# Optimization experiments

Measured on AMD Instinct MI355X. Metric: run time of the kernel, lower is better.

Reference implementation:

```python
import jax, jax.numpy as jnp
import numpy as np

NEIGHBOUR = 3  # matches init_kwargs['neighbour']


def _conv2d(x, w, b=None, stride=1, pad=0):
    out = jax.lax.conv_general_dilated(
        x, w, (stride, stride), [(pad, pad), (pad, pad)],
        dimension_numbers=('NCHW', 'OIHW', 'NCHW'))
    if b is not None:
        out = out + b[None, :, None, None]
    return out


def _warp(x, offset, wg_w, wg_b, conv_w):
    """Deformable bilinear warp: offsets -> 4 corner gathers -> modulate -> regroup -> strided conv."""
    k = NEIGHBOUR
    N = k * k
    B, C, H, W = x.shape
    m = jax.nn.sigmoid(_conv2d(x, wg_w, wg_b, 1, 1))          # [B,N,H,W] modulation gate
    xp = jnp.pad(x, ((0, 0), (0, 0), (1, 1), (1, 1)))         # zero pad -> [B,C,H+2,W+2]
    Hp, Wp = H + 2, W + 2
    r = jnp.arange(-(k - 1) // 2, (k - 1) // 2 + 1, dtype=x.dtype)
    pnx, pny = jnp.meshgrid(r, r, indexing='ij')              # kernel-neighbour offsets p_n
    # absolute sampling positions in padded coords (p_0 starts at 1 due to padding)
    p0x = jnp.arange(1, H + 1, dtype=x.dtype)[None, :, None, None]
    p0y = jnp.arange(1, W + 1, dtype=x.dtype)[None, None, :, None]
    off = offset.transpose(0, 2, 3, 1)                        # [B,H,W,2N]; first N = x, last N = y
    px = p0x + pnx.ravel()[None, None, None, :] + off[..., :N]  # [B,H,W,N]
    py = p0y + pny.ravel()[None, None, None, :] + off[..., N:]
    fx = jnp.floor(jax.lax.stop_gradient(px))                 # p.detach().floor()
    fy = jnp.floor(jax.lax.stop_gradient(py))
    qx_lt = jnp.clip(fx, 0, Hp - 1)
    qy_lt = jnp.clip(fy, 0, Wp - 1)
    qx_rb = jnp.clip(fx + 1, 0, Hp - 1)
    qy_rb = jnp.clip(fy + 1, 0, Wp - 1)
    px = jnp.clip(px, 0, Hp - 1)
    py = jnp.clip(py, 0, Wp - 1)
    # bilinear weights (same algebra as the torch code)
    g_lt = (1 + (qx_lt - px)) * (1 + (qy_lt - py))
    g_rb = (1 - (qx_rb - px)) * (1 - (qy_rb - py))
    g_lb = (1 + (qx_lt - px)) * (1 - (qy_rb - py))
    g_rt = (1 - (qx_rb - px)) * (1 + (qy_lt - py))
    ix_lt = qx_lt.astype(jnp.int32); iy_lt = qy_lt.astype(jnp.int32)
    ix_rb = qx_rb.astype(jnp.int32); iy_rb = qy_rb.astype(jnp.int32)
    x_flat = xp.reshape(B, C, Hp * Wp)

    def gather(ix, iy):
        idx = (ix * Wp + iy).reshape(B, 1, H * W * N)
        return jnp.take_along_axis(x_flat, idx, axis=-1).reshape(B, C, H, W, N)

    xw = (g_lt[:, None] * gather(ix_lt, iy_lt)
          + g_rb[:, None] * gather(ix_rb, iy_rb)
          + g_lb[:, None] * gather(ix_lt, iy_rb)
          + g_rt[:, None] * gather(ix_rb, iy_lt))              # [B,C,H,W,N]
    xw = xw * m.transpose(0, 2, 3, 1)[:, None]                 # modulation, broadcast over C
    # regroup [B,C,H,W,k,k] -> [B,C,H*k,W*k] (matches _reshape_x_warped ordering)
    xw = xw.reshape(B, C, H, W, k, k).transpose(0, 1, 2, 4, 3, 5).reshape(B, C, H * k, W * k)
    return _conv2d(xw, conv_w, None, stride=k, pad=0)          # grouped-back strided conv


def setup_inputs() -> dict:
    B, C, MH, H, W = 4, 64, 18, 128, 128  # MH = 2*neighbour^2
    key = jax.random.key(0)
    ks = jax.random.split(key, 12)
    f32 = jnp.float32
    s = 0.05  # weight scale to keep gates unsaturated
    return {
        'x_t': jax.random.normal(ks[0], (B, C, H, W), f32),
        'pre_offset': jax.random.normal(ks[1], (B, MH, H, W), f32),
        'mean': jax.random.normal(ks[2], (B, MH, H, W), f32),
        'upd_w': s * jax.random.normal(ks[3], (MH, C + MH, 3, 3), f32),
        'upd_b': s * jax.random.normal(ks[4], (MH,), f32),
        'rst_w': s * jax.random.normal(ks[5], (MH, C + MH, 3, 3), f32),
        'rst_b': s * jax.random.normal(ks[6], (MH,), f32),
        'out_w': s * jax.random.normal(ks[7], (MH, C + MH, 3, 3), f32),
        'out_b': s * jax.random.normal(ks[8], (MH,), f32),
        'wg_w': s * jax.random.normal(ks[9], (9, C, 3, 3), f32),
        'wg_b': s * jax.random.normal(ks[10], (9,), f32),
        'warp_conv_w': s * jax.random.normal(ks[11], (C, C, 3, 3), f32),
    }


def reference(x_t, pre_offset, mean, upd_w, upd_b, rst_w, rst_b, out_w, out_b,
              wg_w, wg_b, warp_conv_w):
    stacked = jnp.concatenate([x_t, pre_offset], axis=1)
    update_gate = jax.nn.sigmoid(_conv2d(stacked, upd_w, upd_b, 1, 1))
    reset_gate = jax.nn.sigmoid(_conv2d(stacked, rst_w, rst_b, 1, 1))
    cand = jnp.tanh(_conv2d(jnp.concatenate([x_t, pre_offset * reset_gate], axis=1), out_w, out_b, 1, 1))
    offset = pre_offset * (1 - update_gate) + cand * update_gate
    mean_new = mean + 0.5 * (pre_offset - mean)
    offset = offset + mean_new
    x_out = _warp(x_t, offset, wg_w, wg_b, warp_conv_w)
    return (x_out, offset, mean_new)
```

## Files before the change

kernel.cpp:

```cpp
#include <hip/hip_runtime.h>
#include <hip/hip_bf16.h>
#include <math.h>

#define Bn  4
#define Cc  64
#define MHc 18
#define Hh  128
#define Wd  128
#define HW  (Hh*Wd)
#define Np  9
#define HP  130
#define WP  130
#define XPE (HP*WP*Cc)
#define PPE (HP*WP*32)
#define KX  576
#define KP  288
#define KT  (KX+KP)

typedef __attribute__((ext_vector_type(8))) short short8;
typedef __attribute__((ext_vector_type(4))) float float4v;

__device__ __forceinline__ float bf2f(__hip_bfloat16 x) { return __bfloat162float(x); }
__device__ __forceinline__ __hip_bfloat16 f2bf(float x) { return __float2bfloat16(x); }
__device__ __forceinline__ float sigm(float x) { return 1.f / (1.f + expf(-x)); }
__device__ __forceinline__ float s2f(short s) {
  return __uint_as_float(((unsigned)(unsigned short)s) << 16);
}
__device__ __forceinline__ short f2bs(float x) {
  __hip_bfloat16 h = __float2bfloat16(x);
  return *reinterpret_cast<short*>(&h);
}

#define NW1 (64*KT)
#define NW2 (32*KP)
#define NW3 (Cc*Cc*Np)

__global__ __launch_bounds__(256)
void k_prep(const float* __restrict__ x, const float* __restrict__ po,
            const float* __restrict__ upd_w, const float* __restrict__ rst_w,
            const float* __restrict__ out_w, const float* __restrict__ wg_w,
            const float* __restrict__ wcw,
            __hip_bfloat16* __restrict__ xp, __hip_bfloat16* __restrict__ pp,
            __hip_bfloat16* __restrict__ wall, __hip_bfloat16* __restrict__ w2,
            __hip_bfloat16* __restrict__ wt) {
  __shared__ float tile[16][65];
  int blk = blockIdx.x;
  int t = threadIdx.x;
  if (blk < 4096) {
    int wtile = blk & 7;
    int h = (blk >> 3) & 127;
    int b = blk >> 10;
    int w0 = wtile * 16;
    int wa = t & 15, cq = t >> 4;
    #pragma unroll
    for (int j = 0; j < 4; ++j) {
      int c = cq * 4 + j;
      tile[wa][c] = x[(b*Cc + c)*HW + h*Wd + w0 + wa];
    }
    __syncthreads();
    int cb = t & 63, wq = t >> 6;
    #pragma unroll
    for (int j = 0; j < 4; ++j) {
      int w = wq * 4 + j;
      xp[b*XPE + ((h+1)*WP + (w0 + w + 1))*Cc + cb] = f2bf(tile[w][cb]);
    }
  } else if (blk < 4608) {
    int pb = blk - 4096;
    int h = pb & 127;
    int b = pb >> 7;
    int w = t & 127;
    int half = t >> 7;
    for (int j = 0; j < 9; ++j) {
      int ch = half * 9 + j;
      float v = po[(b*MHc + ch)*HW + h*Wd + w];
      pp[b*PPE + ((h+1)*WP + (w+1))*32 + ch] = f2bf(v);
    }
  } else {
    int idx = (blk - 4608) * 256 + t;
    if (idx < NW1) {
      int k  = idx % KT;
      int gr = idx / KT;
      float v = 0.f;
      if (k < KX) {
        int n = k >> 6, ci = k & 63;
        if      (gr < 18) v = upd_w[(gr*(Cc+MHc) + ci)*9 + n];
        else if (gr < 36) v = rst_w[((gr-18)*(Cc+MHc) + ci)*9 + n];
        else if (gr < 54) v = out_w[((gr-36)*(Cc+MHc) + ci)*9 + n];
        else if (gr < 63) v = wg_w[((gr-54)*Cc + ci)*9 + n];
      } else {
        int kk = k - KX;
        int n = kk >> 5, jc = kk & 31;
        if (jc < 18) {
          if      (gr < 18) v = upd_w[(gr*(Cc+MHc) + Cc + jc)*9 + n];
          else if (gr < 36) v = rst_w[((gr-18)*(Cc+MHc) + Cc + jc)*9 + n];
        }
      }
      wall[idx] = f2bf(v);
    } else if (idx < NW1 + NW2) {
      int i2 = idx - NW1;
      int k  = i2 % KP;
      int oc = i2 / KP;
      int n = k >> 5, jc = k & 31;
      float v = (oc < 18 && jc < 18) ? out_w[(oc*(Cc+MHc) + Cc + jc)*9 + n] : 0.f;
      w2[i2] = f2bf(v);
    } else if (idx < NW1 + NW2 + NW3) {
      int i3 = idx - NW1 - NW2;
      int k  = i3 % 576;
      int co = i3 / 576;
      wt[i3] = f2bf(wcw[(co*Cc + (k & 63))*9 + (k >> 6)]);
    }
  }
}

__global__ __launch_bounds__(256)
void k_gates(const __hip_bfloat16* __restrict__ xpad,
             const __hip_bfloat16* __restrict__ popad,
             const __hip_bfloat16* __restrict__ wall,
             const float* __restrict__ po,
             const float* __restrict__ upd_b,
             const float* __restrict__ rst_b,
             const float* __restrict__ out_b,
             const float* __restrict__ wg_b,
             float* __restrict__ u_out,
             float* __restrict__ cx_out,
             __hip_bfloat16* __restrict__ ropad,
             __hip_bfloat16* __restrict__ m_t) {
  __shared__ __align__(16) char winx[6912];
  __shared__ __align__(16) char winp[3456];
  __shared__ __align__(16) __hip_bfloat16 roL[16][32];
  int blk = blockIdx.x;
  int wtile = blk & 7;
  int h = (blk >> 3) & 127;
  int b = blk >> 10;
  int w0 = wtile * 16;
  int lane = threadIdx.x & 63;
  int wave = threadIdx.x >> 6;
  int t = threadIdx.x;

  ((unsigned int*)roL)[t] = 0u;

  const __hip_bfloat16* xpb = xpad + b * XPE;
  const __hip_bfloat16* ppb = popad + b * PPE;

  for (int i = t; i < 432; i += 256) {
    int r = i / 144, cidx = i - r * 144;
    short8 v = *reinterpret_cast<const short8*>(
        xpb + ((h + r) * WP + w0) * Cc + cidx * 8);
    int o = i * 16;
    *reinterpret_cast<short8*>(winx + (o ^ (((o >> 7) & 7) << 4))) = v;
  }
  if (t < 216) {
    int r = t / 72, cidx = t - r * 72;
    short8 v = *reinterpret_cast<const short8*>(
        ppb + ((h + r) * WP + w0) * 32 + cidx * 8);
    int o = t * 16;
    *reinterpret_cast<short8*>(winp + (o ^ (((o >> 6) & 3) << 4))) = v;
  }
  __syncthreads();

  int mrow = lane & 15;
  int quad = lane >> 4;
  int cotile = wave * 16;
  float4v acc = {0.f, 0.f, 0.f, 0.f};
  #pragma unroll
  for (int ks = 0; ks < KT/32; ++ks) {
    short8 a = *reinterpret_cast<const short8*>(
        wall + (cotile + mrow) * KT + ks * 32 + quad * 8);
    short8 bfr;
    if (ks < 18) {
      int n = ks >> 1;
      int rowidx = (n / 3) * 18 + mrow + (n % 3);
      int lin = rowidx * 128 + (ks & 1) * 64 + quad * 16;
      bfr = *reinterpret_cast<const short8*>(winx + (lin ^ ((rowidx & 7) << 4)));
    } else {
      int n = ks - 18;
      int rowidx = (n / 3) * 18 + mrow + (n % 3);
      int lin = rowidx * 64 + quad * 16;
      bfr = *reinterpret_cast<const short8*>(winp + (lin ^ ((rowidx & 3) << 4)));
    }
    acc = __builtin_amdgcn_mfma_f32_16x16x32_bf16(a, bfr, acc, 0, 0, 0);
  }

  int sp = h * Wd + w0 + mrow;
  #pragma unroll
  for (int r = 0; r < 4; ++r) {
    int gr = cotile + quad * 4 + r;
    float v = acc[r];
    if (gr < 18) {
      u_out[(b*MHc + gr)*HW + sp] = sigm(v + upd_b[gr]);
    } else if (gr < 36) {
      int oc = gr - 18;
      float rr = sigm(v + rst_b[oc]);
      roL[mrow][oc] = f2bf(rr * po[(b*MHc + oc)*HW + sp]);
    } else if (gr < 54) {
      int oc = gr - 36;
      cx_out[(b*MHc + oc)*HW + sp] = v + out_b[oc];
    } else if (gr < 63) {
      int nn = gr - 54;
      m_t[(b*HW + sp)*9 + nn] = f2bf(sigm(v + wg_b[nn]));
    }
  }
  __syncthreads();
  unsigned int* dst = (unsigned int*)(ropad + b*PPE + ((h+1)*WP + (w0+1))*32);
  dst[t] = ((unsigned int*)roL)[t];
}

__global__ __launch_bounds__(256)
void k_fuse(const __hip_bfloat16* __restrict__ xpad,
            const __hip_bfloat16* __restrict__ ropad,
            const __hip_bfloat16* __restrict__ w2,
            const __hip_bfloat16* __restrict__ wt,
            const __hip_bfloat16* __restrict__ m_t,
            const float* __restrict__ po,
            const float* __restrict__ mean,
            float* __restrict__ out_off,
            float* __restrict__ out_mn,
            float* __restrict__ out_x) {
  __shared__ __align__(16) char lbuf[16*584*2];
  __shared__ float offL[16][18];
  __shared__ float mL[16][9];
  __shared__ __align__(16) float gw[144][4];
  __shared__ __align__(16) int   gb[144][2];
  auto xw = (__hip_bfloat16(*)[584])lbuf;

  int blk = blockIdx.x;
  int wtile = blk & 7;
  int h = (blk >> 3) & 127;
  int b = blk >> 10;
  int w0 = wtile * 16;
  int lane = threadIdx.x & 63;
  int wave = threadIdx.x >> 6;
  int t = threadIdx.x;

  const __hip_bfloat16* rpb = ropad + b * PPE;
  if (t < 216) {
    int r = t / 72, cidx = t - r * 72;
    short8 v = *reinterpret_cast<const short8*>(
        rpb + ((h + r) * WP + w0) * 32 + cidx * 8);
    int o = t * 16;
    *reinterpret_cast<short8*>(lbuf + (o ^ (((o >> 6) & 3) << 4))) = v;
  }
  __syncthreads();

  int mrow = lane & 15;
  int quad = lane >> 4;

  if (wave < 2) {
    float4v acc = {0.f, 0.f, 0.f, 0.f};
    #pragma unroll
    for (int ks = 0; ks < KP/32; ++ks) {
      short8 a = *reinterpret_cast<const short8*>(
          w2 + (wave*16 + mrow) * KP + ks * 32 + quad * 8);
      int rowidx = (ks / 3) * 18 + mrow + (ks % 3);
      int lin = rowidx * 64 + quad * 16;
      short8 bfr = *reinterpret_cast<const short8*>(
          lbuf + (lin ^ ((rowidx & 3) << 4)));
      acc = __builtin_amdgcn_mfma_f32_16x16x32_bf16(a, bfr, acc, 0, 0, 0);
    }
    int sp = h * Wd + w0 + mrow;
    #pragma unroll
    for (int r = 0; r < 4; ++r) {
      int gr = wave*16 + quad * 4 + r;
      if (gr < 18) {
        int gi = (b*MHc + gr)*HW + sp;
        float cand = tanhf(out_off[gi] + acc[r]);
        float u = out_mn[gi];
        float p = po[gi];
        float mn = 0.5f * (mean[gi] + p);
        float off = p * (1.f - u) + cand * u + mn;
        out_off[gi] = off;
        out_mn[gi]  = mn;
        offL[mrow][gr] = off;
      }
    }
  } else {
    int base = (wave - 2) * 64 + lane;
    #pragma unroll
    for (int rep = 0; rep < 2; ++rep) {
      int id = base + rep * 128;
      if (id < 144) {
        int px = id / 9, n = id % 9;
        mL[px][n] = bf2f(m_t[(b*HW + h*Wd + w0 + px)*9 + n]);
      }
    }
  }
  __syncthreads();

  if (t < 144) {
    int px = t / 9;
    int n = t - px * 9;
    int wp = w0 + px;
    float ox = offL[px][n];
    float oy = offL[px][9 + n];
    float mnv = mL[px][n];
    float px_ = (float)(h + 1) + (float)(n / 3 - 1) + ox;
    float py_ = (float)(wp + 1) + (float)(n % 3 - 1) + oy;
    float fx = floorf(px_), fy = floorf(py_);
    float xlt = fminf(fmaxf(fx,       0.f), 129.f);
    float ylt = fminf(fmaxf(fy,       0.f), 129.f);
    float xrb = fminf(fmaxf(fx + 1.f, 0.f), 129.f);
    float yrb = fminf(fmaxf(fy + 1.f, 0.f), 129.f);
    float pxc = fminf(fmaxf(px_, 0.f), 129.f);
    float pyc = fminf(fmaxf(py_, 0.f), 129.f);
    float glt = (1.f + xlt - pxc) * (1.f + ylt - pyc);
    float grb = (1.f - xrb + pxc) * (1.f - yrb + pyc);
    float glb = (1.f + xlt - pxc) * (1.f - yrb + pyc);
    float grt = (1.f - xrb + pxc) * (1.f + ylt - pyc);
    int ixl = (int)xlt, iyl = (int)ylt, ixr = (int)xrb, iyr = (int)yrb;
    bool yAdj = (iyr == iyl + 1);
    gw[t][0] = (glt + (yAdj ? 0.f : glb)) * mnv;
    gw[t][1] = (yAdj ? glb : 0.f) * mnv;
    gw[t][2] = (grt + (yAdj ? 0.f : grb)) * mnv;
    gw[t][3] = (yAdj ? grb : 0.f) * mnv;
    gb[t][0] = (ixl * WP + iyl) * Cc;
    gb[t][1] = (ixr * WP + iyl) * Cc;
  }
  __syncthreads();

  const __hip_bfloat16* xpb = xpad + b * XPE;
  for (int it = t; it < 1152; it += 256) {
    int q  = it >> 3;
    int c0 = (it & 7) * 8;
    float4v g = *reinterpret_cast<const float4v*>(gw[q]);
    int bL = gb[q][0], bR = gb[q][1];
    short8 l0 = *reinterpret_cast<const short8*>(xpb + bL + c0);
    short8 l1 = *reinterpret_cast<const short8*>(xpb + bL + 64 + c0);
    short8 r0 = *reinterpret_cast<const short8*>(xpb + bR + c0);
    short8 r1 = *reinterpret_cast<const short8*>(xpb + bR + 64 + c0);
    short8 ov;
    #pragma unroll
    for (int j = 0; j < 8; ++j) {
      float vv = g.x * s2f(l0[j]);
      vv = fmaf(g.y, s2f(l1[j]), vv);
      vv = fmaf(g.z, s2f(r0[j]), vv);
      vv = fmaf(g.w, s2f(r1[j]), vv);
      ov[j] = f2bs(vv);
    }
    int pl = q / 9;
    int n  = q - pl * 9;
    *reinterpret_cast<short8*>(&xw[pl][n * 64 + c0]) = ov;
  }
  __syncthreads();

  int cotile = wave * 16;
  float4v acc = {0.f, 0.f, 0.f, 0.f};
  for (int ks = 0; ks < 18; ++ks) {
    short8 a = *reinterpret_cast<const short8*>(
        wt + (cotile + mrow) * 576 + ks * 32 + quad * 8);
    short8 bfr = *reinterpret_cast<const short8*>(
        &xw[mrow][ks * 32 + quad * 8]);
    acc = __builtin_amdgcn_mfma_f32_16x16x32_bf16(a, bfr, acc, 0, 0, 0);
  }
  #pragma unroll
  for (int r = 0; r < 4; ++r) {
    int co = cotile + quad * 4 + r;
    out_x[((b * Cc + co) * Hh + h) * Wd + w0 + mrow] = acc[r];
  }
}

__global__ void f_convAB(const float* __restrict__ x, const float* __restrict__ po,
                         const float* __restrict__ wA, const float* __restrict__ bA,
                         const float* __restrict__ wB, const float* __restrict__ bB,
                         float* __restrict__ u_scr, float* __restrict__ ro_scr) {
  int idx = blockIdx.x * 256 + threadIdx.x;
  if (idx >= Bn * MHc * HW) return;
  int w = idx & 127, h = (idx >> 7) & 127, oc = (idx >> 14) % MHc, b = idx / (MHc*HW);
  float accA = bA[oc], accB = bB[oc];
  const float* xb = x + b*Cc*HW; const float* pb = po + b*MHc*HW;
  for (int ic = 0; ic < Cc + MHc; ++ic) {
    const float* src = (ic < Cc) ? (xb + ic*HW) : (pb + (ic-Cc)*HW);
    const float* wa = wA + (oc*(Cc+MHc)+ic)*9; const float* wb = wB + (oc*(Cc+MHc)+ic)*9;
    for (int kh = 0; kh < 3; ++kh) { int hh = h+kh-1; if ((unsigned)hh >= Hh) continue;
      for (int kw = 0; kw < 3; ++kw) { int ww = w+kw-1; if ((unsigned)ww >= Wd) continue;
        float v = src[hh*Wd+ww]; accA += v*wa[kh*3+kw]; accB += v*wb[kh*3+kw]; } }
  }
  u_scr[idx] = sigm(accA); ro_scr[idx] = sigm(accB) * pb[oc*HW + h*Wd + w];
}
__global__ void f_convC(const float* __restrict__ x, const float* __restrict__ po,
                        const float* __restrict__ mean, const float* __restrict__ wC,
                        const float* __restrict__ bC, const float* __restrict__ u_scr,
                        const float* __restrict__ ro_scr, float* __restrict__ out_off,
                        float* __restrict__ out_mean) {
  int idx = blockIdx.x * 256 + threadIdx.x;
  if (idx >= Bn * MHc * HW) return;
  int w = idx & 127, h = (idx >> 7) & 127, oc = (idx >> 14) % MHc, b = idx / (MHc*HW);
  float acc = bC[oc];
  const float* xb = x + b*Cc*HW; const float* rb = ro_scr + b*MHc*HW;
  for (int ic = 0; ic < Cc + MHc; ++ic) {
    const float* src = (ic < Cc) ? (xb + ic*HW) : (rb + (ic-Cc)*HW);
    const float* wv = wC + (oc*(Cc+MHc)+ic)*9;
    for (int kh = 0; kh < 3; ++kh) { int hh = h+kh-1; if ((unsigned)hh >= Hh) continue;
      for (int kw = 0; kw < 3; ++kw) { int ww = w+kw-1; if ((unsigned)ww >= Wd) continue;
        acc += src[hh*Wd+ww]*wv[kh*3+kw]; } }
  }
  float cand = tanhf(acc); float u = u_scr[idx]; float p = po[idx];
  float mn = 0.5f*(mean[idx]+p);
  out_off[idx] = p*(1.f-u)+cand*u+mn; out_mean[idx] = mn;
}
__global__ __launch_bounds__(256)
void f_warp(const float* __restrict__ x, const float* __restrict__ off_f,
            const float* __restrict__ wg, const float* __restrict__ bg,
            const float* __restrict__ wc, float* __restrict__ out) {
  __shared__ float mred[4][Np][64]; __shared__ float mval[4][Np];
  __shared__ float xwv[4][Np][64];
  int lane = threadIdx.x & 63, wave = threadIdx.x >> 6;
  int p = blockIdx.x * 4 + wave;
  int b = p >> 14, rem = p & 16383, h = rem >> 7, w = rem & 127;
  const float* xc = x + (b*Cc + lane)*HW;
  float part[Np];
  for (int n = 0; n < Np; ++n) part[n] = 0.f;
  for (int kh = 0; kh < 3; ++kh) { int hh = h+kh-1; if ((unsigned)hh >= Hh) continue;
    for (int kw = 0; kw < 3; ++kw) { int ww = w+kw-1; if ((unsigned)ww >= Wd) continue;
      float v = xc[hh*Wd+ww];
      for (int n = 0; n < Np; ++n) part[n] += v*wg[(n*Cc+lane)*9+kh*3+kw]; } }
  for (int n = 0; n < Np; ++n) mred[wave][n][lane] = part[n];
  __syncthreads();
  if (lane < Np) { float s = bg[lane];
    for (int c = 0; c < Cc; ++c) s += mred[wave][lane][c];
    mval[wave][lane] = sigm(s); }
  __syncthreads();
  const float* offb = off_f + b*MHc*HW; int sp = h*Wd + w;
  for (int n = 0; n < Np; ++n) {
    float px = (float)(h+1) + (float)(n/3-1) + offb[n*HW+sp];
    float py = (float)(w+1) + (float)(n%3-1) + offb[(9+n)*HW+sp];
    float fxq = floorf(px), fyq = floorf(py);
    float xlt = fminf(fmaxf(fxq,0.f),129.f), ylt = fminf(fmaxf(fyq,0.f),129.f);
    float xrb = fminf(fmaxf(fxq+1.f,0.f),129.f), yrb = fminf(fmaxf(fyq+1.f,0.f),129.f);
    float pxc = fminf(fmaxf(px,0.f),129.f), pyc = fminf(fmaxf(py,0.f),129.f);
    float glt = (1.f+xlt-pxc)*(1.f+ylt-pyc), grb = (1.f-xrb+pxc)*(1.f-yrb+pyc);
    float glb = (1.f+xlt-pxc)*(1.f-yrb+pyc), grt = (1.f-xrb+pxc)*(1.f+ylt-pyc);
    int ixl=(int)xlt, iyl=(int)ylt, ixr=(int)xrb, iyr=(int)yrb;
    float vlt=0.f,vrb=0.f,vlb=0.f,vrt=0.f;
    if (ixl>=1&&ixl<=Hh&&iyl>=1&&iyl<=Wd) vlt = xc[(ixl-1)*Wd+(iyl-1)];
    if (ixr>=1&&ixr<=Hh&&iyr>=1&&iyr<=Wd) vrb = xc[(ixr-1)*Wd+(iyr-1)];
    if (ixl>=1&&ixl<=Hh&&iyr>=1&&iyr<=Wd) vlb = xc[(ixl-1)*Wd+(iyr-1)];
    if (ixr>=1&&ixr<=Hh&&iyl>=1&&iyl<=Wd) vrt = xc[(ixr-1)*Wd+(iyl-1)];
    xwv[wave][n][lane] = (glt*vlt+grb*vrb+glb*vlb+grt*vrt)*mval[wave][n];
  }
  __syncthreads();
  float acc = 0.f;
  for (int c = 0; c < Cc; ++c)
    for (int n = 0; n < Np; ++n)
      acc += xwv[wave][n][c]*wc[(lane*Cc+c)*9+n];
  out[(b*Cc+lane)*HW + h*Wd + w] = acc;
}

extern "C" void kernel_launch(void* const* d_in, const int* in_sizes, int n_in,
                              void* d_out, int out_size, void* d_ws, size_t ws_size,
                              hipStream_t stream) {
  (void)in_sizes; (void)n_in; (void)out_size;
  const float* x_t   = (const float*)d_in[0];
  const float* po    = (const float*)d_in[1];
  const float* mean  = (const float*)d_in[2];
  const float* upd_w = (const float*)d_in[3];
  const float* upd_b = (const float*)d_in[4];
  const float* rst_w = (const float*)d_in[5];
  const float* rst_b = (const float*)d_in[6];
  const float* out_w = (const float*)d_in[7];
  const float* out_b = (const float*)d_in[8];
  const float* wg_w  = (const float*)d_in[9];
  const float* wg_b  = (const float*)d_in[10];
  const float* wcw   = (const float*)d_in[11];

  float* out_x   = (float*)d_out;
  float* out_off = out_x + 4194304;
  float* out_mn  = out_off + 1179648;

  char* ws = (char*)d_ws;
  __hip_bfloat16* xpad  = (__hip_bfloat16*)(ws + 0);
  __hip_bfloat16* popad = (__hip_bfloat16*)(ws + 8652800);
  __hip_bfloat16* ropad = (__hip_bfloat16*)(ws + 12979200);
  __hip_bfloat16* wall  = (__hip_bfloat16*)(ws + 17305600);
  __hip_bfloat16* w2    = (__hip_bfloat16*)(ws + 17416192);
  __hip_bfloat16* wt_bf = (__hip_bfloat16*)(ws + 17434624);
  __hip_bfloat16* m_t   = (__hip_bfloat16*)(ws + 17508352);
  const size_t WS_NEED = 18688000;

  if (ws_size >= WS_NEED) {
    hipMemsetAsync(d_ws, 0, 17305600, stream);
    hipLaunchKernelGGL(k_prep,  dim3(5004), dim3(256), 0, stream,
                       x_t, po, upd_w, rst_w, out_w, wg_w, wcw,
                       xpad, popad, wall, w2, wt_bf);
    hipLaunchKernelGGL(k_gates, dim3(4096), dim3(256), 0, stream,
                       xpad, popad, wall, po, upd_b, rst_b, out_b, wg_b,
                       out_mn, out_off, ropad, m_t);
    hipLaunchKernelGGL(k_fuse,  dim3(4096), dim3(256), 0, stream,
                       xpad, ropad, w2, wt_bf, m_t, po, mean,
                       out_off, out_mn, out_x);
  } else {
    float* u_scr  = out_x;
    float* cx_scr = out_x + 1179648;
    hipLaunchKernelGGL(f_convAB, dim3(4608), dim3(256), 0, stream,
                       x_t, po, upd_w, upd_b, rst_w, rst_b, u_scr, cx_scr);
    hipLaunchKernelGGL(f_convC,  dim3(4608), dim3(256), 0, stream,
                       x_t, po, mean, out_w, out_b, u_scr, cx_scr,
                       out_off, out_mn);
    hipLaunchKernelGGL(f_warp,   dim3(16384), dim3(256), 0, stream,
                       x_t, out_off, wg_w, wg_b, wcw, out_x);
  }
}
```

Baseline: 203.1 us.

## Widen prep and gate tiles, vectorize transposes, transpose gate layout, prefetch fuse operands

k_prep now handles a whole 128-pixel row per block, with float4 loads and 16-byte bf16 stores for the NHWC transpose, and batches the pre_offset loads. k_gates computes 32 pixels per block with two MFMA accumulators so each weight fragment is reused twice, and it stores the modulation gate in a planar [9][B*HW] layout. k_fuse prefetches the per-pixel offset, mean and gate operands before the barrier and reads the planar gate with coalesced loads. The aim is fewer blocks, less launch and transpose overhead, and better memory coalescing, at the cost of more LDS per block in k_gates.

Result: faster. 183.8 us (-9.5%).

```diff
diff --git a/kernel.cpp b/kernel.cpp
--- a/kernel.cpp
+++ b/kernel.cpp
@@ -43,40 +43,48 @@
             __hip_bfloat16* __restrict__ xp, __hip_bfloat16* __restrict__ pp,
             __hip_bfloat16* __restrict__ wall, __hip_bfloat16* __restrict__ w2,
             __hip_bfloat16* __restrict__ wt) {
-  __shared__ float tile[16][65];
+  __shared__ float tile[128][65];
   int blk = blockIdx.x;
   int t = threadIdx.x;
-  if (blk < 4096) {
-    int wtile = blk & 7;
-    int h = (blk >> 3) & 127;
-    int b = blk >> 10;
-    int w0 = wtile * 16;
-    int wa = t & 15, cq = t >> 4;
+  if (blk < 512) {
+    int b = blk >> 7, h = blk & 127;
+    int c = t >> 2;
+    int wbase = (t & 3) * 32;
+    const float* src = &x[(b*Cc + c)*HW + h*Wd + wbase];
+    #pragma unroll
+    for (int j = 0; j < 8; ++j) {
+      float4v v = *reinterpret_cast<const float4v*>(src + j*4);
+      tile[wbase + j*4 + 0][c] = v.x;
+      tile[wbase + j*4 + 1][c] = v.y;
+      tile[wbase + j*4 + 2][c] = v.z;
+      tile[wbase + j*4 + 3][c] = v.w;
+    }
+    __syncthreads();
     #pragma unroll
     for (int j = 0; j < 4; ++j) {
-      int c = cq * 4 + j;
-      tile[wa][c] = x[(b*Cc + c)*HW + h*Wd + w0 + wa];
-    }
-    __syncthreads();
-    int cb = t & 63, wq = t >> 6;
-    #pragma unroll
-    for (int j = 0; j < 4; ++j) {
-      int w = wq * 4 + j;
-      xp[b*XPE + ((h+1)*WP + (w0 + w + 1))*Cc + cb] = f2bf(tile[w][cb]);
-    }
-  } else if (blk < 4608) {
-    int pb = blk - 4096;
+      int i = t + j * 256;
+      int px = i >> 3, oct = i & 7;
+      short8 ov;
+      #pragma unroll
+      for (int e = 0; e < 8; ++e) ov[e] = f2bs(tile[px][oct*8 + e]);
+      *reinterpret_cast<short8*>(
+          &xp[b*XPE + ((h+1)*WP + px + 1)*Cc + oct*8]) = ov;
+    }
+  } else if (blk < 1024) {
+    int pb = blk - 512;
     int h = pb & 127;
     int b = pb >> 7;
     int w = t & 127;
     int half = t >> 7;
-    for (int j = 0; j < 9; ++j) {
-      int ch = half * 9 + j;
-      float v = po[(b*MHc + ch)*HW + h*Wd + w];
-      pp[b*PPE + ((h+1)*WP + (w+1))*32 + ch] = f2bf(v);
-    }
+    float v[9];
+    #pragma unroll
+    for (int j = 0; j < 9; ++j)
+      v[j] = po[(b*MHc + half*9 + j)*HW + h*Wd + w];
+    #pragma unroll
+    for (int j = 0; j < 9; ++j)
+      pp[b*PPE + ((h+1)*WP + (w+1))*32 + half*9 + j] = f2bf(v[j]);
   } else {
-    int idx = (blk - 4608) * 256 + t;
+    int idx = (blk - 1024) * 256 + t;
     if (idx < NW1) {
       int k  = idx % KT;
       int gr = idx / KT;
@@ -125,35 +133,36 @@
              float* __restrict__ cx_out,
              __hip_bfloat16* __restrict__ ropad,
              __hip_bfloat16* __restrict__ m_t) {
-  __shared__ __align__(16) char winx[6912];
-  __shared__ __align__(16) char winp[3456];
-  __shared__ __align__(16) __hip_bfloat16 roL[16][32];
+  __shared__ __align__(16) char winx[13056];
+  __shared__ __align__(16) char winp[6528];
+  __shared__ __align__(16) __hip_bfloat16 roL[32][32];
   int blk = blockIdx.x;
-  int wtile = blk & 7;
-  int h = (blk >> 3) & 127;
-  int b = blk >> 10;
-  int w0 = wtile * 16;
+  int wtile = blk & 3;
+  int h = (blk >> 2) & 127;
+  int b = blk >> 9;
+  int w0 = wtile * 32;
   int lane = threadIdx.x & 63;
   int wave = threadIdx.x >> 6;
   int t = threadIdx.x;
 
   ((unsigned int*)roL)[t] = 0u;
+  ((unsigned int*)roL)[t + 256] = 0u;
 
   const __hip_bfloat16* xpb = xpad + b * XPE;
   const __hip_bfloat16* ppb = popad + b * PPE;
 
-  for (int i = t; i < 432; i += 256) {
-    int r = i / 144, cidx = i - r * 144;
+  for (int i = t; i < 816; i += 256) {
+    int r = i / 272, cidx = i - r * 272;
     short8 v = *reinterpret_cast<const short8*>(
         xpb + ((h + r) * WP + w0) * Cc + cidx * 8);
     int o = i * 16;
     *reinterpret_cast<short8*>(winx + (o ^ (((o >> 7) & 7) << 4))) = v;
   }
-  if (t < 216) {
-    int r = t / 72, cidx = t - r * 72;
+  for (int i = t; i < 408; i += 256) {
+    int r = i / 136, cidx = i - r * 136;
     short8 v = *reinterpret_cast<const short8*>(
         ppb + ((h + r) * WP + w0) * 32 + cidx * 8);
-    int o = t * 16;
+    int o = i * 16;
     *reinterpret_cast<short8*>(winp + (o ^ (((o >> 6) & 3) << 4))) = v;
   }
   __syncthreads();
@@ -161,48 +170,70 @@
   int mrow = lane & 15;
   int quad = lane >> 4;
   int cotile = wave * 16;
-  float4v acc = {0.f, 0.f, 0.f, 0.f};
+  float4v acc0 = {0.f, 0.f, 0.f, 0.f};
+  float4v acc1 = {0.f, 0.f, 0.f, 0.f};
   #pragma unroll
   for (int ks = 0; ks < KT/32; ++ks) {
     short8 a = *reinterpret_cast<const short8*>(
         wall + (cotile + mrow) * KT + ks * 32 + quad * 8);
-    short8 bfr;
+    short8 b0, b1;
     if (ks < 18) {
       int n = ks >> 1;
-      int rowidx = (n / 3) * 18 + mrow + (n % 3);
-      int lin = rowidx * 128 + (ks & 1) * 64 + quad * 16;
-      bfr = *reinterpret_cast<const short8*>(winx + (lin ^ ((rowidx & 7) << 4)));
+      int r0i = (n / 3) * 34 + mrow + (n % 3);
+      int r1i = r0i + 16;
+      int l0 = r0i * 128 + (ks & 1) * 64 + quad * 16;
+      int l1 = r1i * 128 + (ks & 1) * 64 + quad * 16;
+      b0 = *reinterpret_cast<const short8*>(winx + (l0 ^ ((r0i & 7) << 4)));
+      b1 = *reinterpret_cast<const short8*>(winx + (l1 ^ ((r1i & 7) << 4)));
     } else {
       int n = ks - 18;
-      int rowidx = (n / 3) * 18 + mrow + (n % 3);
-      int lin = rowidx * 64 + quad * 16;
-      bfr = *reinterpret_cast<const short8*>(winp + (lin ^ ((rowidx & 3) << 4)));
-    }
-    acc = __builtin_amdgcn_mfma_f32_16x16x32_bf16(a, bfr, acc, 0, 0, 0);
-  }
-
-  int sp = h * Wd + w0 + mrow;
+      int r0i = (n / 3) * 34 + mrow + (n % 3);
+      int r1i = r0i + 16;
+      int l0 = r0i * 64 + quad * 16;
+      int l1 = r1i * 64 + quad * 16;
+      b0 = *reinterpret_cast<const short8*>(winp + (l0 ^ ((r0i & 3) << 4)));
+      b1 = *reinterpret_cast<const short8*>(winp + (l1 ^ ((r1i & 3) << 4)));
+    }
+    acc0 = __builtin_amdgcn_mfma_f32_16x16x32_bf16(a, b0, acc0, 0, 0, 0);
+    acc1 = __builtin_amdgcn_mfma_f32_16x16x32_bf16(a, b1, acc1, 0, 0, 0);
+  }
+
+  int sp0 = h * Wd + w0 + mrow;
+  int sp1 = sp0 + 16;
+  float pv0[4], pv1[4];
   #pragma unroll
   for (int r = 0; r < 4; ++r) {
     int gr = cotile + quad * 4 + r;
-    float v = acc[r];
+    if (gr >= 18 && gr < 36) {
+      pv0[r] = po[(b*MHc + (gr-18))*HW + sp0];
+      pv1[r] = po[(b*MHc + (gr-18))*HW + sp1];
+    }
+  }
+  #pragma unroll
+  for (int r = 0; r < 4; ++r) {
+    int gr = cotile + quad * 4 + r;
+    float v0 = acc0[r], v1 = acc1[r];
     if (gr < 18) {
-      u_out[(b*MHc + gr)*HW + sp] = sigm(v + upd_b[gr]);
+      u_out[(b*MHc + gr)*HW + sp0] = sigm(v0 + upd_b[gr]);
+      u_out[(b*MHc + gr)*HW + sp1] = sigm(v1 + upd_b[gr]);
     } else if (gr < 36) {
       int oc = gr - 18;
-      float rr = sigm(v + rst_b[oc]);
-      roL[mrow][oc] = f2bf(rr * po[(b*MHc + oc)*HW + sp]);
+      roL[mrow][oc]      = f2bf(sigm(v0 + rst_b[oc]) * pv0[r]);
+      roL[16 + mrow][oc] = f2bf(sigm(v1 + rst_b[oc]) * pv1[r]);
     } else if (gr < 54) {
       int oc = gr - 36;
-      cx_out[(b*MHc + oc)*HW + sp] = v + out_b[oc];
+      cx_out[(b*MHc + oc)*HW + sp0] = v0 + out_b[oc];
+      cx_out[(b*MHc + oc)*HW + sp1] = v1 + out_b[oc];
     } else if (gr < 63) {
       int nn = gr - 54;
-      m_t[(b*HW + sp)*9 + nn] = f2bf(sigm(v + wg_b[nn]));
+      m_t[nn*(Bn*HW) + b*HW + sp0] = f2bf(sigm(v0 + wg_b[nn]));
+      m_t[nn*(Bn*HW) + b*HW + sp1] = f2bf(sigm(v1 + wg_b[nn]));
     }
   }
   __syncthreads();
   unsigned int* dst = (unsigned int*)(ropad + b*PPE + ((h+1)*WP + (w0+1))*32);
   dst[t] = ((unsigned int*)roL)[t];
+  dst[t + 256] = ((unsigned int*)roL)[t + 256];
 }
 
 __global__ __launch_bounds__(256)
@@ -220,7 +251,7 @@
   __shared__ float offL[16][18];
   __shared__ float mL[16][9];
   __shared__ __align__(16) float gw[144][4];
-  __shared__ __align__(16) int   gb[144][2];
+  __shared__ __align__(16) int   ga[144][2];
   auto xw = (__hip_bfloat16(*)[584])lbuf;
 
   int blk = blockIdx.x;
@@ -232,6 +263,26 @@
   int wave = threadIdx.x >> 6;
   int t = threadIdx.x;
 
+  int mrow = lane & 15;
+  int quad = lane >> 4;
+
+  float ov[4], uv[4], pv[4], mv[4];
+  int gil[4];
+  if (wave < 2) {
+    int sp = h * Wd + w0 + mrow;
+    #pragma unroll
+    for (int r = 0; r < 4; ++r) {
+      int gr = wave*16 + quad * 4 + r;
+      gil[r] = (b*MHc + gr)*HW + sp;
+      if (gr < 18) {
+        ov[r] = out_off[gil[r]];
+        uv[r] = out_mn[gil[r]];
+        pv[r] = po[gil[r]];
+        mv[r] = mean[gil[r]];
+      }
+    }
+  }
+
   const __hip_bfloat16* rpb = ropad + b * PPE;
   if (t < 216) {
     int r = t / 72, cidx = t - r * 72;
@@ -240,10 +291,11 @@
     int o = t * 16;
     *reinterpret_cast<short8*>(lbuf + (o ^ (((o >> 6) & 3) << 4))) = v;
   }
-  __syncthreads();
-
-  int mrow = lane & 15;
-  int quad = lane >> 4;
+  if (t < 144) {
+    int n = t >> 4, px = t & 15;
+    mL[px][n] = bf2f(m_t[n*(Bn*HW) + b*HW + h*Wd + w0 + px]);
+  }
+  __syncthreads();
 
   if (wave < 2) {
     float4v acc = {0.f, 0.f, 0.f, 0.f};
@@ -257,30 +309,16 @@
           lbuf + (lin ^ ((rowidx & 3) << 4)));
       acc = __builtin_amdgcn_mfma_f32_16x16x32_bf16(a, bfr, acc, 0, 0, 0);
     }
-    int sp = h * Wd + w0 + mrow;
     #pragma unroll
     for (int r = 0; r < 4; ++r) {
       int gr = wave*16 + quad * 4 + r;
       if (gr < 18) {
-        int gi = (b*MHc + gr)*HW + sp;
-        float cand = tanhf(out_off[gi] + acc[r]);
-        float u = out_mn[gi];
-        float p = po[gi];
-        float mn = 0.5f * (mean[gi] + p);
-        float off = p * (1.f - u) + cand * u + mn;
-        out_off[gi] = off;
-        out_mn[gi]  = mn;
+        float cand = tanhf(ov[r] + acc[r]);
+        float mn = 0.5f * (mv[r] + pv[r]);
+        float off = pv[r] * (1.f - uv[r]) + cand * uv[r] + mn;
+        out_off[gil[r]] = off;
+        out_mn[gil[r]]  = mn;
         offL[mrow][gr] = off;
-      }
-    }
-  } else {
-    int base = (wave - 2) * 64 + lane;
-    #pragma unroll
-    for (int rep = 0; rep < 2; ++rep) {
-      int id = base + rep * 128;
-      if (id < 144) {
-        int px = id / 9, n = id % 9;
-        mL[px][n] = bf2f(m_t[(b*HW + h*Wd + w0 + px)*9 + n]);
       }
     }
   }
@@ -312,8 +350,8 @@
     gw[t][1] = (yAdj ? glb : 0.f) * mnv;
     gw[t][2] = (grt + (yAdj ? 0.f : grb)) * mnv;
     gw[t][3] = (yAdj ? grb : 0.f) * mnv;
-    gb[t][0] = (ixl * WP + iyl) * Cc;
-    gb[t][1] = (ixr * WP + iyl) * Cc;
+    ga[t][0] = (ixl * WP + iyl) * Cc;
+    ga[t][1] = (ixr * WP + iyl) * Cc;
   }
   __syncthreads();
 
@@ -322,23 +360,23 @@
     int q  = it >> 3;
     int c0 = (it & 7) * 8;
     float4v g = *reinterpret_cast<const float4v*>(gw[q]);
-    int bL = gb[q][0], bR = gb[q][1];
-    short8 l0 = *reinterpret_cast<const short8*>(xpb + bL + c0);
-    short8 l1 = *reinterpret_cast<const short8*>(xpb + bL + 64 + c0);
-    short8 r0 = *reinterpret_cast<const short8*>(xpb + bR + c0);
-    short8 r1 = *reinterpret_cast<const short8*>(xpb + bR + 64 + c0);
-    short8 ov;
+    int bL = ga[q][0] + c0, bR = ga[q][1] + c0;
+    short8 l0 = *reinterpret_cast<const short8*>(xpb + bL);
+    short8 l1 = *reinterpret_cast<const short8*>(xpb + bL + 64);
+    short8 r0 = *reinterpret_cast<const short8*>(xpb + bR);
+    short8 r1 = *reinterpret_cast<const short8*>(xpb + bR + 64);
+    short8 ovv;
     #pragma unroll
     for (int j = 0; j < 8; ++j) {
       float vv = g.x * s2f(l0[j]);
       vv = fmaf(g.y, s2f(l1[j]), vv);
       vv = fmaf(g.z, s2f(r0[j]), vv);
       vv = fmaf(g.w, s2f(r1[j]), vv);
-      ov[j] = f2bs(vv);
+      ovv[j] = f2bs(vv);
     }
     int pl = q / 9;
     int n  = q - pl * 9;
-    *reinterpret_cast<short8*>(&xw[pl][n * 64 + c0]) = ov;
+    *reinterpret_cast<short8*>(&xw[pl][n * 64 + c0]) = ovv;
   }
   __syncthreads();
 
@@ -478,10 +516,10 @@
 
   if (ws_size >= WS_NEED) {
     hipMemsetAsync(d_ws, 0, 17305600, stream);
-    hipLaunchKernelGGL(k_prep,  dim3(5004), dim3(256), 0, stream,
+    hipLaunchKernelGGL(k_prep,  dim3(1420), dim3(256), 0, stream,
                        x_t, po, upd_w, rst_w, out_w, wg_w, wcw,
                        xpad, popad, wall, w2, wt_bf);
-    hipLaunchKernelGGL(k_gates, dim3(4096), dim3(256), 0, stream,
+    hipLaunchKernelGGL(k_gates, dim3(2048), dim3(256), 0, stream,
                        xpad, popad, wall, po, upd_b, rst_b, out_b, wg_b,
                        out_mn, out_off, ropad, m_t);
     hipLaunchKernelGGL(k_fuse,  dim3(4096), dim3(256), 0, stream,
```
